# Optimization experiments

Measured on AMD Instinct MI355X. Metric: run time of the kernel, lower is better.

The kernel has to match this reference:

```python
import jax, jax.numpy as jnp
import numpy as np

B, H, S, D = 2, 16, 2048, 64

def setup_inputs() -> dict:
    key = jax.random.key(0)
    kq, kk, kv = jax.random.split(key, 3)
    q = jax.random.normal(kq, (B, H, S, D), dtype=jnp.float32)
    k = jax.random.normal(kk, (B, H, S, D), dtype=jnp.float32)
    v = jax.random.normal(kv, (B, H, S, D), dtype=jnp.float32)
    return {"q": q, "k": k, "v": v}

def reference(q, k, v):
    d_k = q.shape[-1]
    scale = 1.0 / jnp.sqrt(jnp.asarray(d_k, dtype=q.dtype))
    # scores: [B, H, Sq, Sk]
    scores = jnp.einsum("bhqd,bhkd->bhqk", q, k) * scale
    attn = jax.nn.softmax(scores, axis=-1)
    out = jnp.einsum("bhqk,bhkd->bhqd", attn, v)
    return out
```

## Files before the change

### kernel.cpp

```cpp
#include <hip/hip_runtime.h>
#include <math.h>

constexpr int Bc = 2, Hc = 16, Sc = 2048, Dc = 64;
constexpr int BQ = 128;
constexpr int BK = 64;
constexpr int NT = Sc / BK;

constexpr int KWD = 36;
constexpr int VWD = 33;
constexpr int KSD_OFF = 0;
constexpr int VTD_OFF = 2 * 64 * KWD;
constexpr int SMEM_DW = VTD_OFF + 2 * 64 * VWD;

typedef __attribute__((ext_vector_type(8))) short short8v;
typedef __attribute__((ext_vector_type(4))) float f32x4;
typedef __attribute__((ext_vector_type(4))) unsigned int uint4v;

__device__ __forceinline__ unsigned int cvt_pk_bf16(float lo, float hi) {
    unsigned int d;
    asm("v_cvt_pk_bf16_f32 %0, %1, %2" : "=v"(d) : "v"(lo), "v"(hi));
    return d;
}

__global__ __launch_bounds__(512, 4)
void attn_mfma_kernel(const float* __restrict__ Q,
                      const float* __restrict__ K,
                      const float* __restrict__ V,
                      float* __restrict__ O)
{
    __shared__ __align__(16) unsigned int smem[SMEM_DW];

    const int tid  = threadIdx.x;
    const int wave = tid >> 6;
    const int lane = tid & 63;
    const int n    = lane & 15;
    const int qd   = lane >> 4;
    const int qw   = wave & 3;
    const int kh   = wave >> 2;

    const int hid = blockIdx.x;
    const int hk  = hid >> 3;
    const int bh  = (hid & 7) + 8 * (hk >> 4);
    const int q0  = (hk & 15) * BQ;

    const float* Qg = Q + ((size_t)bh * Sc + q0) * Dc;
    const float* Kg = K + (size_t)bh * Sc * Dc;
    const float* Vg = V + (size_t)bh * Sc * Dc;
    float*       Og = O + ((size_t)bh * Sc + q0) * Dc;

    short8v q_frag[2][2];
#pragma unroll
    for (int qt = 0; qt < 2; ++qt)
#pragma unroll
        for (int kc = 0; kc < 2; ++kc) {
            const float* qrow = Qg + (qw * 32 + qt * 16 + n) * Dc + kc * 32 + qd * 8;
            float4 f0 = *reinterpret_cast<const float4*>(qrow);
            float4 f1 = *reinterpret_cast<const float4*>(qrow + 4);
            uint4v u;
            u[0] = cvt_pk_bf16(f0.x * 0.125f, f0.y * 0.125f);
            u[1] = cvt_pk_bf16(f0.z * 0.125f, f0.w * 0.125f);
            u[2] = cvt_pk_bf16(f1.x * 0.125f, f1.y * 0.125f);
            u[3] = cvt_pk_bf16(f1.z * 0.125f, f1.w * 0.125f);
            q_frag[qt][kc] = __builtin_bit_cast(short8v, u);
        }

    const f32x4 z = {0.f, 0.f, 0.f, 0.f};
    f32x4 o_acc[2][4] = {{z, z, z, z}, {z, z, z, z}};
    float l_part[2] = {0.f, 0.f};

    const int kr  = tid >> 3;
    const int kc8 = (tid & 7) << 3;
    const int vkp = tid >> 4;
    const int dpb = tid & 15;

    const float* kbase = Kg + kr * Dc + kc8;
    const float* vbase = Vg + vkp * 2 * Dc + dpb * 2;

    float4 ka[2];
    float2 va[2], vb[2];

    auto load_regs = [&](int kt) {
        const float* Kt = kbase + kt * (BK * Dc);
        const float* Vt = vbase + kt * (BK * Dc);
        ka[0] = *reinterpret_cast<const float4*>(Kt);
        ka[1] = *reinterpret_cast<const float4*>(Kt + 4);
#pragma unroll
        for (int i = 0; i < 2; ++i) {
            va[i] = *reinterpret_cast<const float2*>(Vt + 32 * i);
            vb[i] = *reinterpret_cast<const float2*>(Vt + Dc + 32 * i);
        }
    };
    auto write_lds = [&](int bb) {
        uint4v w;
        w[0] = cvt_pk_bf16(ka[0].x, ka[0].y);
        w[1] = cvt_pk_bf16(ka[0].z, ka[0].w);
        w[2] = cvt_pk_bf16(ka[1].x, ka[1].y);
        w[3] = cvt_pk_bf16(ka[1].z, ka[1].w);
        *reinterpret_cast<uint4v*>(
            &smem[KSD_OFF + bb * 64 * KWD + kr * KWD + (tid & 7) * 4]) = w;
        unsigned int* vd = &smem[VTD_OFF + bb * 64 * VWD];
#pragma unroll
        for (int i = 0; i < 2; ++i) {
            int dp = dpb + 16 * i;
            vd[(dp * 2)     * VWD + vkp] = cvt_pk_bf16(va[i].x, vb[i].x);
            vd[(dp * 2 + 1) * VWD + vkp] = cvt_pk_bf16(va[i].y, vb[i].y);
        }
    };

    auto compute = [&](int bb) {
        f32x4 st[2][2] = {{z, z}, {z, z}};
        const unsigned int* ks = &smem[KSD_OFF + bb * 64 * KWD];
        __builtin_amdgcn_s_setprio(1);
#pragma unroll
        for (int nt = 0; nt < 2; ++nt)
#pragma unroll
            for (int kc = 0; kc < 2; ++kc) {
                short8v kf = *reinterpret_cast<const short8v*>(
                    &ks[(kh * 32 + nt * 16 + n) * KWD + kc * 16 + qd * 4]);
#pragma unroll
                for (int qt = 0; qt < 2; ++qt)
                    st[qt][nt] = __builtin_amdgcn_mfma_f32_16x16x32_bf16(
                        kf, q_frag[qt][kc], st[qt][nt], 0, 0, 0);
            }
        __builtin_amdgcn_s_setprio(0);

        short8v p_frag[2];
#pragma unroll
        for (int qt = 0; qt < 2; ++qt) {
            float p00 = __expf(st[qt][0][0]), p01 = __expf(st[qt][0][1]);
            float p02 = __expf(st[qt][0][2]), p03 = __expf(st[qt][0][3]);
            float p10 = __expf(st[qt][1][0]), p11 = __expf(st[qt][1][1]);
            float p12 = __expf(st[qt][1][2]), p13 = __expf(st[qt][1][3]);
            l_part[qt] += ((p00 + p01) + (p02 + p03)) + ((p10 + p11) + (p12 + p13));

            unsigned int x0 = cvt_pk_bf16(p00, p01);
            unsigned int x1 = cvt_pk_bf16(p02, p03);
            unsigned int y0 = cvt_pk_bf16(p10, p11);
            unsigned int y1 = cvt_pk_bf16(p12, p13);
            asm("v_permlane32_swap_b32 %0, %1" : "+v"(x0), "+v"(y0));
            asm("v_permlane16_swap_b32 %0, %1" : "+v"(x0), "+v"(y0));
            asm("v_permlane32_swap_b32 %0, %1" : "+v"(x1), "+v"(y1));
            asm("v_permlane16_swap_b32 %0, %1" : "+v"(x1), "+v"(y1));
            uint4v pu; pu[0] = x0; pu[1] = x1; pu[2] = y0; pu[3] = y1;
            p_frag[qt] = __builtin_bit_cast(short8v, pu);
        }

        const unsigned int* vt = &smem[VTD_OFF + bb * 64 * VWD];
        __builtin_amdgcn_s_setprio(1);
#pragma unroll
        for (int dt = 0; dt < 4; ++dt) {
            const unsigned int* vrow = vt + (dt * 16 + n) * VWD + kh * 16 + qd * 4;
            uint4v vu;
            vu[0] = vrow[0]; vu[1] = vrow[1]; vu[2] = vrow[2]; vu[3] = vrow[3];
            short8v vf = __builtin_bit_cast(short8v, vu);
#pragma unroll
            for (int qt = 0; qt < 2; ++qt)
                o_acc[qt][dt] = __builtin_amdgcn_mfma_f32_16x16x32_bf16(
                    p_frag[qt], vf, o_acc[qt][dt], 0, 0, 0);
        }
        __builtin_amdgcn_s_setprio(0);
    };

    load_regs(0);
    write_lds(0);
    __syncthreads();

    int cur = 0;
    for (int kt = 0; kt < NT; ++kt) {
        const bool more = (kt + 1 < NT);
        if (more) load_regs(kt + 1);

        compute(cur);

        if (more) write_lds(cur ^ 1);
        __syncthreads();
        cur ^= 1;
    }

    float* mo = reinterpret_cast<float*>(smem);
    float* ml = reinterpret_cast<float*>(smem + 8192);
    if (kh == 1) {
#pragma unroll
        for (int qt = 0; qt < 2; ++qt) {
#pragma unroll
            for (int dt = 0; dt < 4; ++dt)
                *reinterpret_cast<f32x4*>(
                    &mo[(((qw * 64 + lane) * 2 + qt) * 4 + dt) * 4]) = o_acc[qt][dt];
            ml[(qw * 64 + lane) * 2 + qt] = l_part[qt];
        }
    }
    __syncthreads();
    if (kh == 0) {
#pragma unroll
        for (int qt = 0; qt < 2; ++qt) {
#pragma unroll
            for (int dt = 0; dt < 4; ++dt)
                o_acc[qt][dt] += *reinterpret_cast<const f32x4*>(
                    &mo[(((qw * 64 + lane) * 2 + qt) * 4 + dt) * 4]);
            l_part[qt] += ml[(qw * 64 + lane) * 2 + qt];
        }

#pragma unroll
        for (int qt = 0; qt < 2; ++qt) {
            float lp = l_part[qt];
            lp += __shfl_xor(lp, 16, 64);
            lp += __shfl_xor(lp, 32, 64);
#pragma unroll
            for (int r = 0; r < 4; ++r) {
                float lr  = __shfl(lp, qd * 4 + r, 64);
                float inv = 1.0f / lr;
#pragma unroll
                for (int dt = 0; dt < 4; ++dt) {
                    Og[(qw * 32 + qt * 16 + qd * 4 + r) * Dc + dt * 16 + n] =
                        o_acc[qt][dt][r] * inv;
                }
            }
        }
    }
}

extern "C" void kernel_launch(void* const* d_in, const int* in_sizes, int n_in,
                              void* d_out, int out_size, void* d_ws, size_t ws_size,
                              hipStream_t stream) {
    const float* q = (const float*)d_in[0];
    const float* k = (const float*)d_in[1];
    const float* v = (const float*)d_in[2];
    float*       o = (float*)d_out;

    dim3 grid((Sc / BQ) * Bc * Hc);
    attn_mfma_kernel<<<grid, 512, 0, stream>>>(q, k, v, o);
}
```

Baseline: 131.7 us.

## Load K fragments directly from global into registers, bypassing LDS staging

K tiles are no longer staged through shared memory. Each lane loads its own MFMA K fragments straight from global memory into registers, converts them to bf16 just before the QK^T MFMAs, and prefetches the next tile after those MFMAs. This drops the K LDS writes and reads and shrinks shared memory to the V buffers only. In exchange, K loads are duplicated across the four qw waves that share each kh, raising global/L2 traffic, and the 32-float prefetch buffer raises register pressure under launch_bounds(512,4).

```diff
diff --git a/kernel.cpp b/kernel.cpp
--- a/kernel.cpp
+++ b/kernel.cpp
@@ -6,11 +6,8 @@
 constexpr int BK = 64;
 constexpr int NT = Sc / BK;
 
-constexpr int KWD = 36;
 constexpr int VWD = 33;
-constexpr int KSD_OFF = 0;
-constexpr int VTD_OFF = 2 * 64 * KWD;
-constexpr int SMEM_DW = VTD_OFF + 2 * 64 * VWD;
+constexpr int SMEM_DW = 8832;
 
 typedef __attribute__((ext_vector_type(8))) short short8v;
 typedef __attribute__((ext_vector_type(4))) float f32x4;
@@ -68,37 +65,36 @@
     f32x4 o_acc[2][4] = {{z, z, z, z}, {z, z, z, z}};
     float l_part[2] = {0.f, 0.f};
 
-    const int kr  = tid >> 3;
-    const int kc8 = (tid & 7) << 3;
+    const float* klane = Kg + (kh * 32 + n) * Dc + qd * 8;
+    float4 kpre[2][2][2];
+
     const int vkp = tid >> 4;
     const int dpb = tid & 15;
-
-    const float* kbase = Kg + kr * Dc + kc8;
     const float* vbase = Vg + vkp * 2 * Dc + dpb * 2;
-
-    float4 ka[2];
     float2 va[2], vb[2];
 
-    auto load_regs = [&](int kt) {
-        const float* Kt = kbase + kt * (BK * Dc);
+    auto load_K = [&](int kt) {
+        const float* Kt = klane + kt * (BK * Dc);
+#pragma unroll
+        for (int nt = 0; nt < 2; ++nt)
+#pragma unroll
+            for (int kc = 0; kc < 2; ++kc) {
+                kpre[nt][kc][0] = *reinterpret_cast<const float4*>(
+                    Kt + nt * 16 * Dc + kc * 32);
+                kpre[nt][kc][1] = *reinterpret_cast<const float4*>(
+                    Kt + nt * 16 * Dc + kc * 32 + 4);
+            }
+    };
+    auto load_V = [&](int kt) {
         const float* Vt = vbase + kt * (BK * Dc);
-        ka[0] = *reinterpret_cast<const float4*>(Kt);
-        ka[1] = *reinterpret_cast<const float4*>(Kt + 4);
 #pragma unroll
         for (int i = 0; i < 2; ++i) {
             va[i] = *reinterpret_cast<const float2*>(Vt + 32 * i);
             vb[i] = *reinterpret_cast<const float2*>(Vt + Dc + 32 * i);
         }
     };
-    auto write_lds = [&](int bb) {
-        uint4v w;
-        w[0] = cvt_pk_bf16(ka[0].x, ka[0].y);
-        w[1] = cvt_pk_bf16(ka[0].z, ka[0].w);
-        w[2] = cvt_pk_bf16(ka[1].x, ka[1].y);
-        w[3] = cvt_pk_bf16(ka[1].z, ka[1].w);
-        *reinterpret_cast<uint4v*>(
-            &smem[KSD_OFF + bb * 64 * KWD + kr * KWD + (tid & 7) * 4]) = w;
-        unsigned int* vd = &smem[VTD_OFF + bb * 64 * VWD];
+    auto write_V = [&](int bb) {
+        unsigned int* vd = &smem[bb * 64 * VWD];
 #pragma unroll
         for (int i = 0; i < 2; ++i) {
             int dp = dpb + 16 * i;
@@ -107,22 +103,36 @@
         }
     };
 
-    auto compute = [&](int bb) {
+    load_K(0);
+    load_V(0);
+    write_V(0);
+    __syncthreads();
+
+    int cur = 0;
+    for (int kt = 0; kt < NT; ++kt) {
+        const bool more = (kt + 1 < NT);
+        if (more) load_V(kt + 1);
+
         f32x4 st[2][2] = {{z, z}, {z, z}};
-        const unsigned int* ks = &smem[KSD_OFF + bb * 64 * KWD];
         __builtin_amdgcn_s_setprio(1);
 #pragma unroll
         for (int nt = 0; nt < 2; ++nt)
 #pragma unroll
             for (int kc = 0; kc < 2; ++kc) {
-                short8v kf = *reinterpret_cast<const short8v*>(
-                    &ks[(kh * 32 + nt * 16 + n) * KWD + kc * 16 + qd * 4]);
+                uint4v u;
+                u[0] = cvt_pk_bf16(kpre[nt][kc][0].x, kpre[nt][kc][0].y);
+                u[1] = cvt_pk_bf16(kpre[nt][kc][0].z, kpre[nt][kc][0].w);
+                u[2] = cvt_pk_bf16(kpre[nt][kc][1].x, kpre[nt][kc][1].y);
+                u[3] = cvt_pk_bf16(kpre[nt][kc][1].z, kpre[nt][kc][1].w);
+                short8v kf = __builtin_bit_cast(short8v, u);
 #pragma unroll
                 for (int qt = 0; qt < 2; ++qt)
                     st[qt][nt] = __builtin_amdgcn_mfma_f32_16x16x32_bf16(
                         kf, q_frag[qt][kc], st[qt][nt], 0, 0, 0);
             }
         __builtin_amdgcn_s_setprio(0);
+
+        if (more) load_K(kt + 1);
 
         short8v p_frag[2];
 #pragma unroll
@@ -145,7 +155,7 @@
             p_frag[qt] = __builtin_bit_cast(short8v, pu);
         }
 
-        const unsigned int* vt = &smem[VTD_OFF + bb * 64 * VWD];
+        const unsigned int* vt = &smem[cur * 64 * VWD];
         __builtin_amdgcn_s_setprio(1);
 #pragma unroll
         for (int dt = 0; dt < 4; ++dt) {
@@ -159,20 +169,8 @@
                     p_frag[qt], vf, o_acc[qt][dt], 0, 0, 0);
         }
         __builtin_amdgcn_s_setprio(0);
-    };
-
-    load_regs(0);
-    write_lds(0);
-    __syncthreads();
-
-    int cur = 0;
-    for (int kt = 0; kt < NT; ++kt) {
-        const bool more = (kt + 1 < NT);
-        if (more) load_regs(kt + 1);
-
-        compute(cur);
-
-        if (more) write_lds(cur ^ 1);
+
+        if (more) write_V(cur ^ 1);
         __syncthreads();
         cur ^= 1;
     }
```

New measurement: 214.1 us. 1.63x slower.

## Software-pipeline QK softmax against previous tile's PV with quad-buffered V

Applied to the files above, without the earlier changes.

Splits the per-tile compute into a QK+softmax stage and a PV stage, then skews them so each step runs the QK of tile t alongside the PV of tile t-1. V now has four LDS buffers and K keeps two, and the loop is unrolled by four tiles. The aim is to overlap the exp/convert work with MFMA and hide LDS latency between the dependent stages. In exchange it uses more LDS and more registers for two sets of P fragments, which can lower occupancy.

```diff
diff --git a/kernel.cpp b/kernel.cpp
--- a/kernel.cpp
+++ b/kernel.cpp
@@ -8,9 +8,10 @@
 
 constexpr int KWD = 36;
 constexpr int VWD = 33;
-constexpr int KSD_OFF = 0;
-constexpr int VTD_OFF = 2 * 64 * KWD;
-constexpr int SMEM_DW = VTD_OFF + 2 * 64 * VWD;
+constexpr int KB_STRIDE = 64 * KWD;
+constexpr int VB_STRIDE = 64 * VWD;
+constexpr int VB_OFF    = 2 * KB_STRIDE;
+constexpr int SMEM_DW   = VB_OFF + 4 * VB_STRIDE;
 
 typedef __attribute__((ext_vector_type(8))) short short8v;
 typedef __attribute__((ext_vector_type(4))) float f32x4;
@@ -90,15 +91,15 @@
             vb[i] = *reinterpret_cast<const float2*>(Vt + Dc + 32 * i);
         }
     };
-    auto write_lds = [&](int bb) {
+    auto write_lds = [&](int kb, int vbuf) {
         uint4v w;
         w[0] = cvt_pk_bf16(ka[0].x, ka[0].y);
         w[1] = cvt_pk_bf16(ka[0].z, ka[0].w);
         w[2] = cvt_pk_bf16(ka[1].x, ka[1].y);
         w[3] = cvt_pk_bf16(ka[1].z, ka[1].w);
         *reinterpret_cast<uint4v*>(
-            &smem[KSD_OFF + bb * 64 * KWD + kr * KWD + (tid & 7) * 4]) = w;
-        unsigned int* vd = &smem[VTD_OFF + bb * 64 * VWD];
+            &smem[kb * KB_STRIDE + kr * KWD + (tid & 7) * 4]) = w;
+        unsigned int* vd = &smem[VB_OFF + vbuf * VB_STRIDE];
 #pragma unroll
         for (int i = 0; i < 2; ++i) {
             int dp = dpb + 16 * i;
@@ -107,9 +108,9 @@
         }
     };
 
-    auto compute = [&](int bb) {
+    auto qk_softmax = [&](int kb, short8v* pout) {
         f32x4 st[2][2] = {{z, z}, {z, z}};
-        const unsigned int* ks = &smem[KSD_OFF + bb * 64 * KWD];
+        const unsigned int* ks = &smem[kb * KB_STRIDE];
         __builtin_amdgcn_s_setprio(1);
 #pragma unroll
         for (int nt = 0; nt < 2; ++nt)
@@ -124,7 +125,6 @@
             }
         __builtin_amdgcn_s_setprio(0);
 
-        short8v p_frag[2];
 #pragma unroll
         for (int qt = 0; qt < 2; ++qt) {
             float p00 = __expf(st[qt][0][0]), p01 = __expf(st[qt][0][1]);
@@ -142,10 +142,12 @@
             asm("v_permlane32_swap_b32 %0, %1" : "+v"(x1), "+v"(y1));
             asm("v_permlane16_swap_b32 %0, %1" : "+v"(x1), "+v"(y1));
             uint4v pu; pu[0] = x0; pu[1] = x1; pu[2] = y0; pu[3] = y1;
-            p_frag[qt] = __builtin_bit_cast(short8v, pu);
-        }
-
-        const unsigned int* vt = &smem[VTD_OFF + bb * 64 * VWD];
+            pout[qt] = __builtin_bit_cast(short8v, pu);
+        }
+    };
+
+    auto pv = [&](const short8v* pin, int vbuf) {
+        const unsigned int* vt = &smem[VB_OFF + vbuf * VB_STRIDE];
         __builtin_amdgcn_s_setprio(1);
 #pragma unroll
         for (int dt = 0; dt < 4; ++dt) {
@@ -156,26 +158,42 @@
 #pragma unroll
             for (int qt = 0; qt < 2; ++qt)
                 o_acc[qt][dt] = __builtin_amdgcn_mfma_f32_16x16x32_bf16(
-                    p_frag[qt], vf, o_acc[qt][dt], 0, 0, 0);
+                    pin[qt], vf, o_acc[qt][dt], 0, 0, 0);
         }
         __builtin_amdgcn_s_setprio(0);
     };
 
     load_regs(0);
-    write_lds(0);
+    write_lds(0, 0);
+    load_regs(1);
     __syncthreads();
 
-    int cur = 0;
-    for (int kt = 0; kt < NT; ++kt) {
-        const bool more = (kt + 1 < NT);
-        if (more) load_regs(kt + 1);
-
-        compute(cur);
-
-        if (more) write_lds(cur ^ 1);
-        __syncthreads();
-        cur ^= 1;
+    short8v pA[2], pB[2];
+
+    for (int it = 0; it < NT / 4; ++it) {
+        const int kt0  = it * 4;
+        const bool more = (it + 1 < NT / 4);
+        qk_softmax(0, pA);
+        if (kt0 > 0) pv(pB, 3);
+        write_lds(1, 1);
+        load_regs(kt0 + 2);
+        __syncthreads();
+        qk_softmax(1, pB);
+        pv(pA, 0);
+        write_lds(0, 2);
+        load_regs(kt0 + 3);
+        __syncthreads();
+        qk_softmax(0, pA);
+        pv(pB, 1);
+        write_lds(1, 3);
+        if (more) load_regs(kt0 + 4);
+        __syncthreads();
+        qk_softmax(1, pB);
+        pv(pA, 2);
+        if (more) { write_lds(0, 0); load_regs(kt0 + 5); }
+        __syncthreads();
     }
+    pv(pB, 3);
 
     float* mo = reinterpret_cast<float*>(smem);
     float* ml = reinterpret_cast<float*>(smem + 8192);
```

Result: slower. 237.8 us (+80.6%).

## Software-pipeline PV MFMA one tile behind QK and prefetch two tiles ahead

Applied to the files above, without the earlier changes.

Restructures the main loop so the P·V matmul for tile kt-1 is issued right after the QK^T matmul for tile kt, which lets the exp/softmax VALU work overlap with MFMA. Global loads now prefetch two tiles ahead, and V gets a 4-deep LDS ring with a zeroed dummy slot for the first iteration. The aim is to hide exp latency and global load latency behind matrix work. In exchange it uses more LDS and more registers, which could lower occupancy, and it adds a redundant clamped load near the end of the loop.

```diff
diff --git a/kernel.cpp b/kernel.cpp
--- a/kernel.cpp
+++ b/kernel.cpp
@@ -8,9 +8,10 @@
 
 constexpr int KWD = 36;
 constexpr int VWD = 33;
-constexpr int KSD_OFF = 0;
-constexpr int VTD_OFF = 2 * 64 * KWD;
-constexpr int SMEM_DW = VTD_OFF + 2 * 64 * VWD;
+constexpr int KB_STRIDE = 64 * KWD;
+constexpr int VB_STRIDE = 64 * VWD;
+constexpr int VB_OFF    = 2 * KB_STRIDE;
+constexpr int SMEM_DW   = VB_OFF + 4 * VB_STRIDE;
 
 typedef __attribute__((ext_vector_type(8))) short short8v;
 typedef __attribute__((ext_vector_type(4))) float f32x4;
@@ -76,40 +77,51 @@
     const float* kbase = Kg + kr * Dc + kc8;
     const float* vbase = Vg + vkp * 2 * Dc + dpb * 2;
 
-    float4 ka[2];
-    float2 va[2], vb[2];
-
-    auto load_regs = [&](int kt) {
-        const float* Kt = kbase + kt * (BK * Dc);
-        const float* Vt = vbase + kt * (BK * Dc);
-        ka[0] = *reinterpret_cast<const float4*>(Kt);
-        ka[1] = *reinterpret_cast<const float4*>(Kt + 4);
-#pragma unroll
-        for (int i = 0; i < 2; ++i) {
-            va[i] = *reinterpret_cast<const float2*>(Vt + 32 * i);
-            vb[i] = *reinterpret_cast<const float2*>(Vt + Dc + 32 * i);
-        }
-    };
-    auto write_lds = [&](int bb) {
+    float4 ka0, ka1;
+    float2 va0, va1, vb0, vb1;
+
+    {
+        const float* Kt = kbase;
+        const float* Vt = vbase;
+        ka0 = *reinterpret_cast<const float4*>(Kt);
+        ka1 = *reinterpret_cast<const float4*>(Kt + 4);
+        va0 = *reinterpret_cast<const float2*>(Vt);
+        vb0 = *reinterpret_cast<const float2*>(Vt + Dc);
+        va1 = *reinterpret_cast<const float2*>(Vt + 32);
+        vb1 = *reinterpret_cast<const float2*>(Vt + Dc + 32);
+    }
+    {
         uint4v w;
-        w[0] = cvt_pk_bf16(ka[0].x, ka[0].y);
-        w[1] = cvt_pk_bf16(ka[0].z, ka[0].w);
-        w[2] = cvt_pk_bf16(ka[1].x, ka[1].y);
-        w[3] = cvt_pk_bf16(ka[1].z, ka[1].w);
-        *reinterpret_cast<uint4v*>(
-            &smem[KSD_OFF + bb * 64 * KWD + kr * KWD + (tid & 7) * 4]) = w;
-        unsigned int* vd = &smem[VTD_OFF + bb * 64 * VWD];
-#pragma unroll
-        for (int i = 0; i < 2; ++i) {
-            int dp = dpb + 16 * i;
-            vd[(dp * 2)     * VWD + vkp] = cvt_pk_bf16(va[i].x, vb[i].x);
-            vd[(dp * 2 + 1) * VWD + vkp] = cvt_pk_bf16(va[i].y, vb[i].y);
-        }
-    };
-
-    auto compute = [&](int bb) {
+        w[0] = cvt_pk_bf16(ka0.x, ka0.y);
+        w[1] = cvt_pk_bf16(ka0.z, ka0.w);
+        w[2] = cvt_pk_bf16(ka1.x, ka1.y);
+        w[3] = cvt_pk_bf16(ka1.z, ka1.w);
+        *reinterpret_cast<uint4v*>(&smem[kr * KWD + (tid & 7) * 4]) = w;
+        unsigned int* vd = &smem[VB_OFF];
+        vd[(dpb * 2)            * VWD + vkp] = cvt_pk_bf16(va0.x, vb0.x);
+        vd[(dpb * 2 + 1)        * VWD + vkp] = cvt_pk_bf16(va0.y, vb0.y);
+        vd[((dpb + 16) * 2)     * VWD + vkp] = cvt_pk_bf16(va1.x, vb1.x);
+        vd[((dpb + 16) * 2 + 1) * VWD + vkp] = cvt_pk_bf16(va1.y, vb1.y);
+    }
+    {
+        const float* Kt = kbase + BK * Dc;
+        const float* Vt = vbase + BK * Dc;
+        ka0 = *reinterpret_cast<const float4*>(Kt);
+        ka1 = *reinterpret_cast<const float4*>(Kt + 4);
+        va0 = *reinterpret_cast<const float2*>(Vt);
+        vb0 = *reinterpret_cast<const float2*>(Vt + Dc);
+        va1 = *reinterpret_cast<const float2*>(Vt + 32);
+        vb1 = *reinterpret_cast<const float2*>(Vt + Dc + 32);
+    }
+    for (int i = tid; i < VB_STRIDE; i += 512)
+        smem[VB_OFF + 3 * VB_STRIDE + i] = 0u;
+    __syncthreads();
+
+    short8v pp0 = {0,0,0,0,0,0,0,0}, pp1 = {0,0,0,0,0,0,0,0};
+
+    for (int kt = 0; kt < NT; ++kt) {
+        const unsigned int* ks = &smem[(kt & 1) * KB_STRIDE];
         f32x4 st[2][2] = {{z, z}, {z, z}};
-        const unsigned int* ks = &smem[KSD_OFF + bb * 64 * KWD];
         __builtin_amdgcn_s_setprio(1);
 #pragma unroll
         for (int nt = 0; nt < 2; ++nt)
@@ -124,7 +136,24 @@
             }
         __builtin_amdgcn_s_setprio(0);
 
-        short8v p_frag[2];
+        {
+            const unsigned int* vt = &smem[VB_OFF + ((kt - 1) & 3) * VB_STRIDE];
+            __builtin_amdgcn_s_setprio(1);
+#pragma unroll
+            for (int dt = 0; dt < 4; ++dt) {
+                const unsigned int* vrow = vt + (dt * 16 + n) * VWD + kh * 16 + qd * 4;
+                uint4v vu;
+                vu[0] = vrow[0]; vu[1] = vrow[1]; vu[2] = vrow[2]; vu[3] = vrow[3];
+                short8v vf = __builtin_bit_cast(short8v, vu);
+                o_acc[0][dt] = __builtin_amdgcn_mfma_f32_16x16x32_bf16(
+                    pp0, vf, o_acc[0][dt], 0, 0, 0);
+                o_acc[1][dt] = __builtin_amdgcn_mfma_f32_16x16x32_bf16(
+                    pp1, vf, o_acc[1][dt], 0, 0, 0);
+            }
+            __builtin_amdgcn_s_setprio(0);
+        }
+
+        short8v pc0, pc1;
 #pragma unroll
         for (int qt = 0; qt < 2; ++qt) {
             float p00 = __expf(st[qt][0][0]), p01 = __expf(st[qt][0][1]);
@@ -142,43 +171,59 @@
             asm("v_permlane32_swap_b32 %0, %1" : "+v"(x1), "+v"(y1));
             asm("v_permlane16_swap_b32 %0, %1" : "+v"(x1), "+v"(y1));
             uint4v pu; pu[0] = x0; pu[1] = x1; pu[2] = y0; pu[3] = y1;
-            p_frag[qt] = __builtin_bit_cast(short8v, pu);
-        }
-
-        const unsigned int* vt = &smem[VTD_OFF + bb * 64 * VWD];
-        __builtin_amdgcn_s_setprio(1);
+            if (qt == 0) pc0 = __builtin_bit_cast(short8v, pu);
+            else         pc1 = __builtin_bit_cast(short8v, pu);
+        }
+
+        {
+            uint4v w;
+            w[0] = cvt_pk_bf16(ka0.x, ka0.y);
+            w[1] = cvt_pk_bf16(ka0.z, ka0.w);
+            w[2] = cvt_pk_bf16(ka1.x, ka1.y);
+            w[3] = cvt_pk_bf16(ka1.z, ka1.w);
+            *reinterpret_cast<uint4v*>(
+                &smem[((kt + 1) & 1) * KB_STRIDE + kr * KWD + (tid & 7) * 4]) = w;
+            unsigned int* vd = &smem[VB_OFF + ((kt + 1) & 3) * VB_STRIDE];
+            vd[(dpb * 2)            * VWD + vkp] = cvt_pk_bf16(va0.x, vb0.x);
+            vd[(dpb * 2 + 1)        * VWD + vkp] = cvt_pk_bf16(va0.y, vb0.y);
+            vd[((dpb + 16) * 2)     * VWD + vkp] = cvt_pk_bf16(va1.x, vb1.x);
+            vd[((dpb + 16) * 2 + 1) * VWD + vkp] = cvt_pk_bf16(va1.y, vb1.y);
+        }
+
+        {
+            const int lt = (kt + 2 < NT) ? kt + 2 : NT - 1;
+            const float* Kt = kbase + lt * (BK * Dc);
+            const float* Vt = vbase + lt * (BK * Dc);
+            ka0 = *reinterpret_cast<const float4*>(Kt);
+            ka1 = *reinterpret_cast<const float4*>(Kt + 4);
+            va0 = *reinterpret_cast<const float2*>(Vt);
+            vb0 = *reinterpret_cast<const float2*>(Vt + Dc);
+            va1 = *reinterpret_cast<const float2*>(Vt + 32);
+            vb1 = *reinterpret_cast<const float2*>(Vt + Dc + 32);
+        }
+
+        __syncthreads();
+        pp0 = pc0; pp1 = pc1;
+    }
+
+    {
+        const unsigned int* vt = &smem[VB_OFF + ((NT - 1) & 3) * VB_STRIDE];
 #pragma unroll
         for (int dt = 0; dt < 4; ++dt) {
             const unsigned int* vrow = vt + (dt * 16 + n) * VWD + kh * 16 + qd * 4;
             uint4v vu;
             vu[0] = vrow[0]; vu[1] = vrow[1]; vu[2] = vrow[2]; vu[3] = vrow[3];
             short8v vf = __builtin_bit_cast(short8v, vu);
-#pragma unroll
-            for (int qt = 0; qt < 2; ++qt)
-                o_acc[qt][dt] = __builtin_amdgcn_mfma_f32_16x16x32_bf16(
-                    p_frag[qt], vf, o_acc[qt][dt], 0, 0, 0);
-        }
-        __builtin_amdgcn_s_setprio(0);
-    };
-
-    load_regs(0);
-    write_lds(0);
-    __syncthreads();
-
-    int cur = 0;
-    for (int kt = 0; kt < NT; ++kt) {
-        const bool more = (kt + 1 < NT);
-        if (more) load_regs(kt + 1);
-
-        compute(cur);
-
-        if (more) write_lds(cur ^ 1);
-        __syncthreads();
-        cur ^= 1;
+            o_acc[0][dt] = __builtin_amdgcn_mfma_f32_16x16x32_bf16(
+                pp0, vf, o_acc[0][dt], 0, 0, 0);
+            o_acc[1][dt] = __builtin_amdgcn_mfma_f32_16x16x32_bf16(
+                pp1, vf, o_acc[1][dt], 0, 0, 0);
+        }
     }
 
     float* mo = reinterpret_cast<float*>(smem);
     float* ml = reinterpret_cast<float*>(smem + 8192);
+    __syncthreads();
     if (kh == 1) {
 #pragma unroll
         for (int qt = 0; qt < 2; ++qt) {
```

New measurement: 132.6 us. About the same (+0.7%).
